# Optimization experiments

Measured on AMD Instinct MI355X. Metric: run time of the kernel, lower is better.

## Reference

```python
import jax, jax.numpy as jnp
import numpy as np

B, T, C = 2, 2048, 2048
H = 16
D = C // H  # head_dim = 128


def setup_inputs() -> dict:
    key = jax.random.key(0)
    ks = jax.random.split(key, 7)
    scale = C ** -0.5
    x = jax.random.normal(ks[0], (B, T, C), dtype=jnp.float32)
    padding_mask = jax.random.randint(ks[1], (B, T), 0, 2, dtype=jnp.int32)
    Wq = jax.random.normal(ks[2], (C, C), dtype=jnp.float32) * scale
    Wk = jax.random.normal(ks[3], (C, C), dtype=jnp.float32) * scale
    Wv = jax.random.normal(ks[4], (C, C), dtype=jnp.float32) * scale
    Wp = jax.random.normal(ks[5], (C, C), dtype=jnp.float32) * scale
    bp = jax.random.normal(ks[6], (C,), dtype=jnp.float32) * 0.01
    return {"x": x, "padding_mask": padding_mask, "Wq": Wq, "Wk": Wk,
            "Wv": Wv, "Wp": Wp, "bp": bp}


def reference(x, padding_mask, Wq, Wk, Wv, Wp, bp):
    b, t, c = x.shape
    # projections (nn.Linear: x @ W.T), split heads -> [B,H,T,D]
    q = (x @ Wq.T).reshape(b, t, H, D).transpose(0, 2, 1, 3)
    k = (x @ Wk.T).reshape(b, t, H, D).transpose(0, 2, 1, 3)
    v = (x @ Wv.T).reshape(b, t, H, D).transpose(0, 2, 1, 3)
    scores = jnp.einsum('bhtd,bhsd->bhts', q, k) * (D ** -0.5)  # [B,H,T,T]
    # padding mask broadcasts along query rows: pm[b,i] masks row i (as in torch source)
    scores = jnp.where(padding_mask[:, None, :, None] == 0, jnp.float32(-1e9), scores)
    # causal mask
    causal = jnp.tril(jnp.ones((t, t), dtype=bool))
    scores = jnp.where(causal, scores, -jnp.inf)
    attn = jax.nn.softmax(scores, axis=-1)
    ctx = jnp.einsum('bhts,bhsd->bhtd', attn, v)
    ctx = ctx.transpose(0, 2, 1, 3).reshape(b, t, c)
    return ctx @ Wp.T + bp
```

## Files before the change

kernel.cpp:

```cpp
#include <hip/hip_runtime.h>
#include <stdint.h>

typedef __attribute__((ext_vector_type(8))) short vshort8;
typedef __attribute__((ext_vector_type(4))) short vshort4;
typedef __attribute__((ext_vector_type(4))) float vfloat4;

__device__ __forceinline__ short f2bf(float f) {
  union { float f; uint32_t u; } v; v.f = f;
  uint32_t r = (v.u + 0x7FFFu + ((v.u >> 16) & 1u)) >> 16;
  return (short)r;
}
__device__ __forceinline__ void gl_lds16(const void* g, void* l) {
  __builtin_amdgcn_global_load_lds(
      (const __attribute__((address_space(1))) void*)g,
      (__attribute__((address_space(3))) void*)l, 16, 0, 0);
}

__global__ void cvt_kernel(const float* __restrict__ src, short* __restrict__ dst,
                           int n) {
  int i = (blockIdx.x * blockDim.x + threadIdx.x) * 8;
  if (i >= n) return;
  vfloat4 a = *(const vfloat4*)(src + i);
  vfloat4 b = *(const vfloat4*)(src + i + 4);
  vshort8 o;
#pragma unroll
  for (int j = 0; j < 4; ++j) { o[j] = f2bf(a[j]); o[j + 4] = f2bf(b[j]); }
  *(vshort8*)(dst + i) = o;
}

__global__ void cvt3_kernel(const float* __restrict__ s0, const float* __restrict__ s1,
                            const float* __restrict__ s2, short* __restrict__ dst, int n) {
  const float* s = (blockIdx.y == 0) ? s0 : ((blockIdx.y == 1) ? s1 : s2);
  int i = (blockIdx.x * blockDim.x + threadIdx.x) * 8;
  if (i >= n) return;
  vfloat4 a = *(const vfloat4*)(s + i);
  vfloat4 b = *(const vfloat4*)(s + i + 4);
  vshort8 o;
#pragma unroll
  for (int j = 0; j < 4; ++j) { o[j] = f2bf(a[j]); o[j + 4] = f2bf(b[j]); }
  *(vshort8*)(dst + (size_t)blockIdx.y * n + i) = o;
}

__global__ __launch_bounds__(256) void gemm_qkv(
    const short* __restrict__ A, const short* __restrict__ Wcat,
    short* __restrict__ Qw, short* __restrict__ Kw, short* __restrict__ Vtw,
    int M, int K, float scale) {
  __shared__ __attribute__((aligned(16))) short As[128 * 32];
  __shared__ __attribute__((aligned(16))) short Bs[128 * 32];

  const int tid  = threadIdx.x;
  const int lane = tid & 63;
  const int w    = tid >> 6;
  const int lrow = lane & 15;
  const int quad = lane >> 4;
  const int wm   = (w & 1) * 64;
  const int wn   = (w >> 1) * 64;
  const int m0   = blockIdx.y * 128;
  const int n0   = blockIdx.x * 128;
  const int sw   = (lrow >> 1) & 3;

  vfloat4 acc[4][4] = {};

  for (int k0 = 0; k0 < K; k0 += 32) {
    __syncthreads();
#pragma unroll
    for (int i = 0; i < 2; ++i) {
      int c = tid + i * 256;
      int row = c >> 2;
      int s8  = c & 3;
      int g8  = s8 ^ ((row >> 1) & 3);
      gl_lds16(A + ((size_t)(m0 + row) * K + k0 + g8 * 8), (void*)(As + c * 8));
      gl_lds16(Wcat + ((size_t)(n0 + row) * K + k0 + g8 * 8), (void*)(Bs + c * 8));
    }
    __syncthreads();
    vshort8 af[4], bfr[4];
#pragma unroll
    for (int mt = 0; mt < 4; ++mt)
      af[mt] = *(const vshort8*)(As + (wm + mt * 16 + lrow) * 32 + (quad ^ sw) * 8);
#pragma unroll
    for (int nt = 0; nt < 4; ++nt)
      bfr[nt] = *(const vshort8*)(Bs + (wn + nt * 16 + lrow) * 32 + (quad ^ sw) * 8);
#pragma unroll
    for (int mt = 0; mt < 4; ++mt)
#pragma unroll
      for (int nt = 0; nt < 4; ++nt)
        acc[mt][nt] = __builtin_amdgcn_mfma_f32_16x16x32_bf16(af[mt], bfr[nt], acc[mt][nt], 0, 0, 0);
  }

  const int region = n0 >> 11;
#pragma unroll
  for (int mt = 0; mt < 4; ++mt) {
    int mbase = m0 + wm + mt * 16 + quad * 4;
#pragma unroll
    for (int nt = 0; nt < 4; ++nt) {
      int ng = n0 + wn + nt * 16 + lrow;
      int nn = ng & 2047;
      if (region == 2) {
        vshort4 sv;
#pragma unroll
        for (int r = 0; r < 4; ++r) sv[r] = f2bf(acc[mt][nt][r]);
        *(vshort4*)(Vtw + (size_t)nn * 4096 + mbase) = sv;
      } else if (region == 0) {
#pragma unroll
        for (int r = 0; r < 4; ++r)
          Qw[(size_t)(mbase + r) * 2048 + nn] = f2bf(acc[mt][nt][r] * scale);
      } else {
#pragma unroll
        for (int r = 0; r < 4; ++r)
          Kw[(size_t)(mbase + r) * 2048 + nn] = f2bf(acc[mt][nt][r]);
      }
    }
  }
}

__global__ __launch_bounds__(256) void gemm_proj(
    const short* __restrict__ A, const short* __restrict__ B,
    float* __restrict__ C, const float* __restrict__ bias,
    int M, int K, int ldC) {
  __shared__ __attribute__((aligned(16))) short As[128 * 32];
  __shared__ __attribute__((aligned(16))) short Bs[128 * 32];

  const int tid  = threadIdx.x;
  const int lane = tid & 63;
  const int w    = tid >> 6;
  const int lrow = lane & 15;
  const int quad = lane >> 4;
  const int wm   = (w & 1) * 64;
  const int wn   = (w >> 1) * 64;
  const int m0   = blockIdx.y * 128;
  const int n0   = blockIdx.x * 128;
  const int sw   = (lrow >> 1) & 3;

  vfloat4 acc[4][4] = {};

  for (int k0 = 0; k0 < K; k0 += 32) {
    __syncthreads();
#pragma unroll
    for (int i = 0; i < 2; ++i) {
      int c = tid + i * 256;
      int row = c >> 2;
      int s8  = c & 3;
      int g8  = s8 ^ ((row >> 1) & 3);
      gl_lds16(A + ((size_t)(m0 + row) * K + k0 + g8 * 8), (void*)(As + c * 8));
      gl_lds16(B + ((size_t)(n0 + row) * K + k0 + g8 * 8), (void*)(Bs + c * 8));
    }
    __syncthreads();
    vshort8 af[4], bfr[4];
#pragma unroll
    for (int mt = 0; mt < 4; ++mt)
      af[mt] = *(const vshort8*)(As + (wm + mt * 16 + lrow) * 32 + (quad ^ sw) * 8);
#pragma unroll
    for (int nt = 0; nt < 4; ++nt)
      bfr[nt] = *(const vshort8*)(Bs + (wn + nt * 16 + lrow) * 32 + (quad ^ sw) * 8);
#pragma unroll
    for (int mt = 0; mt < 4; ++mt)
#pragma unroll
      for (int nt = 0; nt < 4; ++nt)
        acc[mt][nt] = __builtin_amdgcn_mfma_f32_16x16x32_bf16(af[mt], bfr[nt], acc[mt][nt], 0, 0, 0);
  }

#pragma unroll
  for (int mt = 0; mt < 4; ++mt) {
    int mbase = m0 + wm + mt * 16 + quad * 4;
#pragma unroll
    for (int nt = 0; nt < 4; ++nt) {
      int n = n0 + wn + nt * 16 + lrow;
      float badd = bias[n];
#pragma unroll
      for (int r = 0; r < 4; ++r)
        C[(size_t)(mbase + r) * ldC + n] = acc[mt][nt][r] + badd;
    }
  }
}

__global__ __launch_bounds__(256) void attn_kernel(
    const short* __restrict__ Q, const short* __restrict__ Kg,
    const short* __restrict__ Vt, const int* __restrict__ pm,
    short* __restrict__ ctx) {
  const int T = 2048, Cd = 2048, D = 128, MT = 4096;
  __shared__ __attribute__((aligned(16))) short Ks[64][136];
  __shared__ __attribute__((aligned(16))) short Vs[144][72];
  __shared__ __attribute__((aligned(16))) short Ps[4][16][72];

  const int tid  = threadIdx.x;
  const int lane = tid & 63;
  const int w    = tid >> 6;
  const int lrow = lane & 15;
  const int quad = lane >> 4;
  const int p = blockIdx.x, h = blockIdx.y, b = blockIdx.z;

  for (int i = tid; i < 16 * 72; i += 256) {
    int rr = i / 72, cc = i % 72;
    Vs[128 + rr][cc] = (rr == 0) ? (short)0x3F80 : (short)0;
  }

#pragma unroll 1
  for (int tt = 0; tt < 2; ++tt) {
    const int qt = tt ? (31 - p) : p;
    const int q0 = qt * 64;
    const int qrow = q0 + w * 16 + quad * 4;

    vshort8 qf[4];
#pragma unroll
    for (int ks = 0; ks < 4; ++ks)
      qf[ks] = *(const vshort8*)(Q + (size_t)(b * T + q0 + w * 16 + lrow) * Cd +
                                 h * D + ks * 32 + quad * 8);
    bool keep[4];
#pragma unroll
    for (int r = 0; r < 4; ++r) keep[r] = pm[b * T + qrow + r] != 0;

    vfloat4 oacc[8] = {};
    vfloat4 osum = {};

    __syncthreads();
#pragma unroll
    for (int i = 0; i < 4; ++i) {
      int c = tid + i * 256;
      int kr = c >> 4, kc = c & 15;
      *(vfloat4*)(&Ks[kr][kc * 8]) =
          *(const vfloat4*)(Kg + (size_t)(b * T + kr) * Cd + h * D + kc * 8);
      int vr = c >> 3, vc = c & 7;
      *(vfloat4*)(&Vs[vr][vc * 8]) =
          *(const vfloat4*)(Vt + (size_t)(h * D + vr) * MT + b * T + vc * 8);
    }
    __syncthreads();

#pragma unroll 1
    for (int j = 0; j <= qt; ++j) {
      const int jn = (j < qt) ? (j + 1) : qt;
      vfloat4 pk[4], pv[4];
#pragma unroll
      for (int i = 0; i < 4; ++i) {
        int c = tid + i * 256;
        int kr = c >> 4, kc = c & 15;
        pk[i] = *(const vfloat4*)(Kg + (size_t)(b * T + jn * 64 + kr) * Cd + h * D + kc * 8);
        int vr = c >> 3, vc = c & 7;
        pv[i] = *(const vfloat4*)(Vt + (size_t)(h * D + vr) * MT + b * T + jn * 64 + vc * 8);
      }

      vfloat4 sacc[4] = {};
#pragma unroll
      for (int nt = 0; nt < 4; ++nt)
#pragma unroll
        for (int ks = 0; ks < 4; ++ks) {
          vshort8 kf = *(const vshort8*)(&Ks[nt * 16 + lrow][ks * 32 + quad * 8]);
          sacc[nt] = __builtin_amdgcn_mfma_f32_16x16x32_bf16(qf[ks], kf, sacc[nt], 0, 0, 0);
        }

#pragma unroll
      for (int nt = 0; nt < 4; ++nt) {
        int s_idx = j * 64 + nt * 16 + lrow;
#pragma unroll
        for (int r = 0; r < 4; ++r) {
          float sv = keep[r] ? sacc[nt][r] : 0.0f;
          float pe = __expf(sv - 12.0f);
          pe = (s_idx <= qrow + r) ? pe : 0.0f;
          Ps[w][quad * 4 + r][nt * 16 + lrow] = f2bf(pe);
        }
      }

      vshort8 pf[2];
#pragma unroll
      for (int kp = 0; kp < 2; ++kp)
        pf[kp] = *(const vshort8*)(&Ps[w][lrow][kp * 32 + quad * 8]);
#pragma unroll
      for (int dt = 0; dt < 8; ++dt)
#pragma unroll
        for (int kp = 0; kp < 2; ++kp) {
          vshort8 vf = *(const vshort8*)(&Vs[dt * 16 + lrow][kp * 32 + quad * 8]);
          oacc[dt] = __builtin_amdgcn_mfma_f32_16x16x32_bf16(pf[kp], vf, oacc[dt], 0, 0, 0);
        }
#pragma unroll
      for (int kp = 0; kp < 2; ++kp) {
        vshort8 vf = *(const vshort8*)(&Vs[128 + lrow][kp * 32 + quad * 8]);
        osum = __builtin_amdgcn_mfma_f32_16x16x32_bf16(pf[kp], vf, osum, 0, 0, 0);
      }

      __syncthreads();
#pragma unroll
      for (int i = 0; i < 4; ++i) {
        int c = tid + i * 256;
        int kr = c >> 4, kc = c & 15;
        *(vfloat4*)(&Ks[kr][kc * 8]) = pk[i];
        int vr = c >> 3, vc = c & 7;
        *(vfloat4*)(&Vs[vr][vc * 8]) = pv[i];
      }
      __syncthreads();
    }

    float l[4];
#pragma unroll
    for (int r = 0; r < 4; ++r)
      l[r] = fmaxf(__shfl(osum[r], (lane & 48), 64), 1e-30f);

#pragma unroll
    for (int dt = 0; dt < 8; ++dt) {
      int d = dt * 16 + lrow;
#pragma unroll
      for (int r = 0; r < 4; ++r) {
        float o = oacc[dt][r] / l[r];
        ctx[(size_t)(b * T + qrow + r) * Cd + h * D + d] = f2bf(o);
      }
    }
  }
}

extern "C" void kernel_launch(void* const* d_in, const int* in_sizes, int n_in,
                              void* d_out, int out_size, void* d_ws, size_t ws_size,
                              hipStream_t stream) {
  (void)in_sizes; (void)n_in; (void)out_size; (void)ws_size;
  const float* x  = (const float*)d_in[0];
  const int*   pm = (const int*)d_in[1];
  const float* Wq = (const float*)d_in[2];
  const float* Wk = (const float*)d_in[3];
  const float* Wv = (const float*)d_in[4];
  const float* Wp = (const float*)d_in[5];
  const float* bp = (const float*)d_in[6];
  float* out = (float*)d_out;

  const int Bb = 2, T = 2048, Cd = 2048, M = Bb * T;
  const size_t SZ = (size_t)M * Cd;
  const size_t WZ = (size_t)Cd * Cd;
  short* xb   = (short*)d_ws;
  short* Qw   = xb + SZ;
  short* Kw   = Qw + SZ;
  short* Vtw  = Kw + SZ;
  short* Cx   = Vtw + SZ;
  short* wcat = Cx + SZ;

  const int CB = 256;
  dim3 gx(((int)SZ / 8 + CB - 1) / CB);
  dim3 gw(((int)WZ / 8 + CB - 1) / CB);
  const float scale = 0.08838834764831845f;

  cvt_kernel<<<gx, CB, 0, stream>>>(x, xb, (int)SZ);
  cvt3_kernel<<<dim3(gw.x, 3), CB, 0, stream>>>(Wq, Wk, Wv, wcat, (int)WZ);

  gemm_qkv<<<dim3(6144 / 128, M / 128), 256, 0, stream>>>(
      xb, wcat, Qw, Kw, Vtw, M, Cd, scale);

  attn_kernel<<<dim3(16, 16, Bb), 256, 0, stream>>>(Qw, Kw, Vtw, pm, Cx);

  cvt_kernel<<<gw, CB, 0, stream>>>(Wp, wcat, (int)WZ);
  gemm_proj<<<dim3(Cd / 128, M / 128), 256, 0, stream>>>(Cx, wcat, out, bp, M, Cd, Cd);
}
```

Measured before the change: 423.2 us.

## Rewrite QKV and projection GEMMs with triple-buffered async LDS pipeline and larger tiles

Replaces the single-buffered 128x128, k=32 GEMM loop with a shared macro that uses 128x256 tiles, 512 threads (8 waves) and a k-step of 64. Operands are staged through three LDS buffers, with global-to-LDS loads issued two tiles ahead. Explicit vmcnt/lgkmcnt waits, s_barrier and setprio interleave the loads with the MFMA work. The aim is to hide global memory latency and cut barrier overhead per unit of compute. In exchange it uses about 144KB of LDS per block, which limits occupancy to one block per CU, and it relies on hand-counted wait values being correct.

```diff
diff --git a/kernel.cpp b/kernel.cpp
--- a/kernel.cpp
+++ b/kernel.cpp
@@ -41,134 +41,149 @@
   *(vshort8*)(dst + (size_t)blockIdx.y * n + i) = o;
 }
 
-__global__ __launch_bounds__(256) void gemm_qkv(
-    const short* __restrict__ A, const short* __restrict__ Wcat,
+#define GEMM_MAIN_LOOP()                                                        \
+  const int tid  = threadIdx.x;                                                 \
+  const int lane = tid & 63;                                                    \
+  const int w    = tid >> 6;                                                    \
+  const int wr   = w >> 2;                                                      \
+  const int wc   = w & 3;                                                       \
+  const int lrow = lane & 15;                                                   \
+  const int quad = lane >> 4;                                                   \
+  const int swz  = lrow & 7;                                                    \
+  const int m0   = blockIdx.y * 128;                                            \
+  const int n0   = blockIdx.x * 256;                                            \
+  const int rr   = tid >> 3;                                                    \
+  const int cg8  = ((tid & 7) ^ ((tid >> 3) & 7)) * 8;                          \
+  const short* Ag = Aptr + (size_t)(m0 + rr) * K + cg8;                         \
+  const short* Bg = Bptr + (size_t)(n0 + rr) * K + cg8;                         \
+  auto stageA = [&](int bb, int kt, int i) {                                    \
+    gl_lds16(Ag + (size_t)i * 64 * K + (size_t)kt * 64,                         \
+             (void*)&lds[bb][i * 4096 + tid * 8]);                              \
+  };                                                                            \
+  auto stageB = [&](int bb, int kt, int i) {                                    \
+    gl_lds16(Bg + (size_t)i * 64 * K + (size_t)kt * 64,                         \
+             (void*)&lds[bb][8192 + i * 4096 + tid * 8]);                       \
+  };                                                                            \
+  const int aoff = (wr * 64 + lrow) * 64;                                       \
+  const int boff = (wc * 64 + lrow) * 64;                                       \
+  const int g8a0 = (quad ^ swz) * 8;                                            \
+  const int g8a1 = ((4 + quad) ^ swz) * 8;                                      \
+  vfloat4 acc[4][4] = {};                                                       \
+  const int NT = K >> 6;                                                        \
+                        \
+  stageA(0, 0, 0); stageA(0, 0, 1);                                             \
+  stageB(0, 0, 0); stageB(0, 0, 1); stageB(0, 0, 2); stageB(0, 0, 3);           \
+  stageA(1, 1, 0); stageA(1, 1, 1);                                             \
+  stageB(1, 1, 0); stageB(1, 1, 1); stageB(1, 1, 2); stageB(1, 1, 3);           \
+  int cbuf = 0;                                                                 \
+  for (int t = 0; t < NT; ++t) {                                                \
+    const short* As = lds[cbuf];                                                \
+    const short* Bs = lds[cbuf] + 8192;                                         \
+    const int sb = (cbuf == 0) ? 2 : cbuf - 1;            \
+                          \
+    if (t + 2 < NT) {                                                           \
+      stageA(sb, t + 2, 0); stageA(sb, t + 2, 1); stageB(sb, t + 2, 0);         \
+      asm volatile("s_waitcnt vmcnt(9)" ::: "memory");                          \
+    } else if (t + 1 < NT) {                                                    \
+      asm volatile("s_waitcnt vmcnt(6)" ::: "memory");                          \
+    } else {                                                                    \
+      asm volatile("s_waitcnt vmcnt(0)" ::: "memory");                          \
+    }                                                                           \
+    __builtin_amdgcn_s_barrier();                                               \
+    __builtin_amdgcn_sched_barrier(0);                                          \
+                                       \
+    vshort8 a0[2][2], b[4][2];                                                  \
+    _Pragma("unroll") for (int mi = 0; mi < 2; ++mi) {                          \
+      a0[mi][0] = *(const vshort8*)(As + aoff + mi * 1024 + g8a0);              \
+      a0[mi][1] = *(const vshort8*)(As + aoff + mi * 1024 + g8a1);              \
+    }                                                                           \
+    _Pragma("unroll") for (int ni = 0; ni < 4; ++ni) {                          \
+      b[ni][0] = *(const vshort8*)(Bs + boff + ni * 1024 + g8a0);               \
+      b[ni][1] = *(const vshort8*)(Bs + boff + ni * 1024 + g8a1);               \
+    }                                                                           \
+    asm volatile("s_waitcnt lgkmcnt(0)" ::: "memory");                          \
+    __builtin_amdgcn_sched_barrier(0);                                          \
+    __builtin_amdgcn_s_setprio(1);                                              \
+    _Pragma("unroll") for (int mi = 0; mi < 2; ++mi)                            \
+      _Pragma("unroll") for (int ni = 0; ni < 4; ++ni)                          \
+        _Pragma("unroll") for (int ks = 0; ks < 2; ++ks)                        \
+          acc[mi][ni] = __builtin_amdgcn_mfma_f32_16x16x32_bf16(                \
+              a0[mi][ks], b[ni][ks], acc[mi][ni], 0, 0, 0);                     \
+    __builtin_amdgcn_s_setprio(0);                                              \
+    __builtin_amdgcn_s_barrier();                                               \
+                                       \
+    vshort8 a1[2][2];                                                           \
+    _Pragma("unroll") for (int mi = 0; mi < 2; ++mi) {                          \
+      a1[mi][0] = *(const vshort8*)(As + aoff + (2 + mi) * 1024 + g8a0);        \
+      a1[mi][1] = *(const vshort8*)(As + aoff + (2 + mi) * 1024 + g8a1);        \
+    }                                                                           \
+    if (t + 2 < NT) {                                                           \
+      stageB(sb, t + 2, 1); stageB(sb, t + 2, 2); stageB(sb, t + 2, 3);         \
+    }                                                                           \
+    asm volatile("s_waitcnt lgkmcnt(0)" ::: "memory");                          \
+    __builtin_amdgcn_sched_barrier(0);                                          \
+    __builtin_amdgcn_s_setprio(1);                                              \
+    _Pragma("unroll") for (int mi = 0; mi < 2; ++mi)                            \
+      _Pragma("unroll") for (int ni = 0; ni < 4; ++ni)                          \
+        _Pragma("unroll") for (int ks = 0; ks < 2; ++ks)                        \
+          acc[2 + mi][ni] = __builtin_amdgcn_mfma_f32_16x16x32_bf16(            \
+              a1[mi][ks], b[ni][ks], acc[2 + mi][ni], 0, 0, 0);                 \
+    __builtin_amdgcn_s_setprio(0);                                              \
+    __builtin_amdgcn_s_barrier();                                               \
+    __builtin_amdgcn_sched_barrier(0);                                          \
+    cbuf = (cbuf == 2) ? 0 : cbuf + 1;                                          \
+  }
+
+__global__ __launch_bounds__(512, 2) void gemm_qkv(
+    const short* __restrict__ Aptr, const short* __restrict__ Bptr,
     short* __restrict__ Qw, short* __restrict__ Kw, short* __restrict__ Vtw,
     int M, int K, float scale) {
-  __shared__ __attribute__((aligned(16))) short As[128 * 32];
-  __shared__ __attribute__((aligned(16))) short Bs[128 * 32];
-
-  const int tid  = threadIdx.x;
-  const int lane = tid & 63;
-  const int w    = tid >> 6;
-  const int lrow = lane & 15;
-  const int quad = lane >> 4;
-  const int wm   = (w & 1) * 64;
-  const int wn   = (w >> 1) * 64;
-  const int m0   = blockIdx.y * 128;
-  const int n0   = blockIdx.x * 128;
-  const int sw   = (lrow >> 1) & 3;
-
-  vfloat4 acc[4][4] = {};
-
-  for (int k0 = 0; k0 < K; k0 += 32) {
-    __syncthreads();
-#pragma unroll
-    for (int i = 0; i < 2; ++i) {
-      int c = tid + i * 256;
-      int row = c >> 2;
-      int s8  = c & 3;
-      int g8  = s8 ^ ((row >> 1) & 3);
-      gl_lds16(A + ((size_t)(m0 + row) * K + k0 + g8 * 8), (void*)(As + c * 8));
-      gl_lds16(Wcat + ((size_t)(n0 + row) * K + k0 + g8 * 8), (void*)(Bs + c * 8));
-    }
-    __syncthreads();
-    vshort8 af[4], bfr[4];
-#pragma unroll
-    for (int mt = 0; mt < 4; ++mt)
-      af[mt] = *(const vshort8*)(As + (wm + mt * 16 + lrow) * 32 + (quad ^ sw) * 8);
-#pragma unroll
-    for (int nt = 0; nt < 4; ++nt)
-      bfr[nt] = *(const vshort8*)(Bs + (wn + nt * 16 + lrow) * 32 + (quad ^ sw) * 8);
-#pragma unroll
-    for (int mt = 0; mt < 4; ++mt)
-#pragma unroll
-      for (int nt = 0; nt < 4; ++nt)
-        acc[mt][nt] = __builtin_amdgcn_mfma_f32_16x16x32_bf16(af[mt], bfr[nt], acc[mt][nt], 0, 0, 0);
-  }
+  __shared__ __attribute__((aligned(16))) short lds[3][24576];
+  GEMM_MAIN_LOOP()
 
   const int region = n0 >> 11;
 #pragma unroll
-  for (int mt = 0; mt < 4; ++mt) {
-    int mbase = m0 + wm + mt * 16 + quad * 4;
-#pragma unroll
-    for (int nt = 0; nt < 4; ++nt) {
-      int ng = n0 + wn + nt * 16 + lrow;
+  for (int mi = 0; mi < 4; ++mi) {
+    int mbase = m0 + wr * 64 + mi * 16 + quad * 4;
+#pragma unroll
+    for (int ni = 0; ni < 4; ++ni) {
+      int ng = n0 + wc * 64 + ni * 16 + lrow;
       int nn = ng & 2047;
       if (region == 2) {
         vshort4 sv;
 #pragma unroll
-        for (int r = 0; r < 4; ++r) sv[r] = f2bf(acc[mt][nt][r]);
+        for (int r = 0; r < 4; ++r) sv[r] = f2bf(acc[mi][ni][r]);
         *(vshort4*)(Vtw + (size_t)nn * 4096 + mbase) = sv;
       } else if (region == 0) {
 #pragma unroll
         for (int r = 0; r < 4; ++r)
-          Qw[(size_t)(mbase + r) * 2048 + nn] = f2bf(acc[mt][nt][r] * scale);
+          Qw[(size_t)(mbase + r) * 2048 + nn] = f2bf(acc[mi][ni][r] * scale);
       } else {
 #pragma unroll
         for (int r = 0; r < 4; ++r)
-          Kw[(size_t)(mbase + r) * 2048 + nn] = f2bf(acc[mt][nt][r]);
-      }
-    }
-  }
-}
-
-__global__ __launch_bounds__(256) void gemm_proj(
-    const short* __restrict__ A, const short* __restrict__ B,
+          Kw[(size_t)(mbase + r) * 2048 + nn] = f2bf(acc[mi][ni][r]);
+      }
+    }
+  }
+}
+
+__global__ __launch_bounds__(512, 2) void gemm_proj(
+    const short* __restrict__ Aptr, const short* __restrict__ Bptr,
     float* __restrict__ C, const float* __restrict__ bias,
     int M, int K, int ldC) {
-  __shared__ __attribute__((aligned(16))) short As[128 * 32];
-  __shared__ __attribute__((aligned(16))) short Bs[128 * 32];
-
-  const int tid  = threadIdx.x;
-  const int lane = tid & 63;
-  const int w    = tid >> 6;
-  const int lrow = lane & 15;
-  const int quad = lane >> 4;
-  const int wm   = (w & 1) * 64;
-  const int wn   = (w >> 1) * 64;
-  const int m0   = blockIdx.y * 128;
-  const int n0   = blockIdx.x * 128;
-  const int sw   = (lrow >> 1) & 3;
-
-  vfloat4 acc[4][4] = {};
-
-  for (int k0 = 0; k0 < K; k0 += 32) {
-    __syncthreads();
-#pragma unroll
-    for (int i = 0; i < 2; ++i) {
-      int c = tid + i * 256;
-      int row = c >> 2;
-      int s8  = c & 3;
-      int g8  = s8 ^ ((row >> 1) & 3);
-      gl_lds16(A + ((size_t)(m0 + row) * K + k0 + g8 * 8), (void*)(As + c * 8));
-      gl_lds16(B + ((size_t)(n0 + row) * K + k0 + g8 * 8), (void*)(Bs + c * 8));
-    }
-    __syncthreads();
-    vshort8 af[4], bfr[4];
-#pragma unroll
-    for (int mt = 0; mt < 4; ++mt)
-      af[mt] = *(const vshort8*)(As + (wm + mt * 16 + lrow) * 32 + (quad ^ sw) * 8);
-#pragma unroll
-    for (int nt = 0; nt < 4; ++nt)
-      bfr[nt] = *(const vshort8*)(Bs + (wn + nt * 16 + lrow) * 32 + (quad ^ sw) * 8);
-#pragma unroll
-    for (int mt = 0; mt < 4; ++mt)
-#pragma unroll
-      for (int nt = 0; nt < 4; ++nt)
-        acc[mt][nt] = __builtin_amdgcn_mfma_f32_16x16x32_bf16(af[mt], bfr[nt], acc[mt][nt], 0, 0, 0);
-  }
-
-#pragma unroll
-  for (int mt = 0; mt < 4; ++mt) {
-    int mbase = m0 + wm + mt * 16 + quad * 4;
-#pragma unroll
-    for (int nt = 0; nt < 4; ++nt) {
-      int n = n0 + wn + nt * 16 + lrow;
+  __shared__ __attribute__((aligned(16))) short lds[3][24576];
+  GEMM_MAIN_LOOP()
+
+#pragma unroll
+  for (int mi = 0; mi < 4; ++mi) {
+    int mbase = m0 + wr * 64 + mi * 16 + quad * 4;
+#pragma unroll
+    for (int ni = 0; ni < 4; ++ni) {
+      int n = n0 + wc * 64 + ni * 16 + lrow;
       float badd = bias[n];
 #pragma unroll
       for (int r = 0; r < 4; ++r)
-        C[(size_t)(mbase + r) * ldC + n] = acc[mt][nt][r] + badd;
+        C[(size_t)(mbase + r) * ldC + n] = acc[mi][ni][r] + badd;
     }
   }
 }
@@ -336,11 +351,11 @@
   cvt_kernel<<<gx, CB, 0, stream>>>(x, xb, (int)SZ);
   cvt3_kernel<<<dim3(gw.x, 3), CB, 0, stream>>>(Wq, Wk, Wv, wcat, (int)WZ);
 
-  gemm_qkv<<<dim3(6144 / 128, M / 128), 256, 0, stream>>>(
+  gemm_qkv<<<dim3(6144 / 256, M / 128), 512, 0, stream>>>(
       xb, wcat, Qw, Kw, Vtw, M, Cd, scale);
 
   attn_kernel<<<dim3(16, 16, Bb), 256, 0, stream>>>(Qw, Kw, Vtw, pm, Cx);
 
   cvt_kernel<<<gw, CB, 0, stream>>>(Wp, wcat, (int)WZ);
-  gemm_proj<<<dim3(Cd / 128, M / 128), 256, 0, stream>>>(Cx, wcat, out, bp, M, Cd, Cd);
-}
+  gemm_proj<<<dim3(Cd / 256, M / 128), 512, 0, stream>>>(Cx, wcat, out, bp, M, Cd, Cd);
+}
```

After: 379.1 us. 1.12x faster.
